# Kernel optimization log

Hardware: AMD Instinct MI355X
Metric: run time of the kernel (lower is better)

The kernel has to match this reference:

```python
import jax, jax.numpy as jnp
import numpy as np

HEIGHT = 8  # output crop height (module init arg)


def setup_inputs() -> dict:
    key = jax.random.key(0)
    k = jax.random.split(key, 8)
    N, Himg, Wimg, C = 16, 512, 512, 3
    M = 8192  # total boxes across the batch
    images = jax.random.normal(k[0], (N, Himg, Wimg, C), jnp.float32)
    feature_map = jax.random.normal(k[1], (N, 128, 128, 32), jnp.float32)
    # boxes: (x1, y1, x2, y2, angle); sized so width = HEIGHT*bw/bh <= 60 < max_width=64
    x1 = jax.random.uniform(k[2], (M,), minval=0.0, maxval=392.0)
    y1 = jax.random.uniform(k[3], (M,), minval=0.0, maxval=448.0)
    bw = jax.random.uniform(k[4], (M,), minval=16.0, maxval=120.0)
    bh = jax.random.uniform(k[5], (M,), minval=16.0, maxval=64.0)
    ang = jax.random.uniform(k[6], (M,), minval=-0.785, maxval=0.785)
    boxes = jnp.stack([x1, y1, x1 + bw, y1 + bh, ang], axis=-1)
    box_indices = jax.random.randint(k[7], (M,), 0, N).astype(jnp.int32)
    return {"images": images, "feature_map": feature_map, "boxes": boxes,
            "box_indices": box_indices, "max_width": 64}


def _roi_rotate(images, boxes, box_indices, max_width):
    """Rotated crop-and-resize with bilinear sampling.
    Returns crops [M, HEIGHT, max_width, C] (zero-padded past each box's width)
    and the per-box float output widths [M]."""
    Himg, Wimg = images.shape[1], images.shape[2]
    x1, y1, x2, y2, ang = (boxes[:, i] for i in range(5))
    bw, bh = x2 - x1, y2 - y1
    width = HEIGHT * bw / bh                      # per-box output width (float)
    cx, cy = (x1 + x2) * 0.5, (y1 + y2) * 0.5     # box center
    s = (bh / HEIGHT)[:, None, None]              # uniform scale (src px per dst px)

    ii = jnp.arange(HEIGHT, dtype=images.dtype)[None, :, None]      # [1,H,1]
    jj = jnp.arange(max_width, dtype=images.dtype)[None, None, :]   # [1,1,W]
    w_ = width[:, None, None]
    dx = s * (jj - (w_ - 1.0) * 0.5)              # [M,H,W] local offsets
    dy = s * (ii - (HEIGHT - 1.0) * 0.5)
    ca = jnp.cos(ang)[:, None, None]
    sa = jnp.sin(ang)[:, None, None]
    sx = cx[:, None, None] + ca * dx - sa * dy    # rotated source coords
    sy = cy[:, None, None] + sa * dx + ca * dy

    x0 = jnp.floor(sx)
    y0 = jnp.floor(sy)
    fx = (sx - x0)[..., None]
    fy = (sy - y0)[..., None]
    x0i = jnp.clip(x0, 0, Wimg - 1).astype(jnp.int32)
    x1i = jnp.clip(x0 + 1.0, 0, Wimg - 1).astype(jnp.int32)
    y0i = jnp.clip(y0, 0, Himg - 1).astype(jnp.int32)
    y1i = jnp.clip(y0 + 1.0, 0, Himg - 1).astype(jnp.int32)

    b = box_indices[:, None, None]                # [M,1,1] broadcasts to [M,H,W]
    v00 = images[b, y0i, x0i]                     # [M,H,W,C] irregular gathers
    v01 = images[b, y0i, x1i]
    v10 = images[b, y1i, x0i]
    v11 = images[b, y1i, x1i]
    out = (v00 * (1 - fx) * (1 - fy) + v01 * fx * (1 - fy)
           + v10 * (1 - fx) * fy + v11 * fx * fy)

    # zero outside the image and past each box's actual width (padding)
    valid = ((jj < jnp.ceil(w_)) & (sx >= 0) & (sx <= Wimg - 1)
             & (sy >= 0) & (sy <= Himg - 1))
    crops = out * valid[..., None].astype(out.dtype)
    return crops, width


def reference(images, feature_map, boxes, box_indices, max_width):
    # feature_map is accepted (forward signature) but, per the source, crops
    # are taken from `images`.
    crops, width = _roi_rotate(images, boxes, box_indices, max_width)
    boxes_padded_width = max_width - width
    return crops, boxes_padded_width
```

## Files before the change

kernel.cpp:

```cpp
#include <hip/hip_runtime.h>

#define HEIGHT 8

__global__ void __launch_bounds__(512)
roi_rotate_kernel(const float* __restrict__ images,
                  const float* __restrict__ boxes,
                  const int* __restrict__ box_indices,
                  float* __restrict__ crops,
                  float* __restrict__ width_out,
                  int max_width, int Himg, int Wimg)
{
    const int m   = blockIdx.x;
    const int tid = threadIdx.x;
    const int mw  = max_width;

    const float x1  = boxes[m * 5 + 0];
    const float y1  = boxes[m * 5 + 1];
    const float x2  = boxes[m * 5 + 2];
    const float y2  = boxes[m * 5 + 3];
    const float ang = boxes[m * 5 + 4];
    const float bwd = x2 - x1, bhd = y2 - y1;
    const float width = (float)HEIGHT * bwd / bhd;
    const float cx = (x1 + x2) * 0.5f;
    const float cy = (y1 + y2) * 0.5f;
    const float s  = bhd / (float)HEIGHT;
    const float ca = cosf(ang);
    const float sa = sinf(ang);

    if (tid == 0) width_out[m] = (float)mw - width;

    const int i = tid & (HEIGHT - 1);
    const int j = tid >> 3;

    const float dx = s * ((float)j - (width - 1.0f) * 0.5f);
    const float dy = s * ((float)i - ((float)HEIGHT - 1.0f) * 0.5f);
    const float sx = cx + ca * dx - sa * dy;
    const float sy = cy + sa * dx + ca * dy;

    float v0 = 0.0f, v1 = 0.0f, v2 = 0.0f;

    const bool valid = ((float)j < ceilf(width)) &&
                       (sx >= 0.0f) && (sx <= (float)(Wimg - 1)) &&
                       (sy >= 0.0f) && (sy <= (float)(Himg - 1));

    if (valid) {
        const float x0 = floorf(sx);
        const float y0 = floorf(sy);
        const float fx = sx - x0;
        const float fy = sy - y0;
        const int x0i = (int)fminf(fmaxf(x0,        0.0f), (float)(Wimg - 1));
        const int x1i = (int)fminf(fmaxf(x0 + 1.0f, 0.0f), (float)(Wimg - 1));
        const int y0i = (int)fminf(fmaxf(y0,        0.0f), (float)(Himg - 1));
        const int y1i = (int)fminf(fmaxf(y0 + 1.0f, 0.0f), (float)(Himg - 1));

        const int b = box_indices[m];
        const float* img = images + (size_t)b * Himg * Wimg * 3;
        const size_t o00 = ((size_t)y0i * Wimg + x0i) * 3;
        const size_t o01 = ((size_t)y0i * Wimg + x1i) * 3;
        const size_t o10 = ((size_t)y1i * Wimg + x0i) * 3;
        const size_t o11 = ((size_t)y1i * Wimg + x1i) * 3;

        const float w00 = (1.0f - fx) * (1.0f - fy);
        const float w01 = fx * (1.0f - fy);
        const float w10 = (1.0f - fx) * fy;
        const float w11 = fx * fy;

        v0 = img[o00 + 0] * w00 + img[o01 + 0] * w01 +
             img[o10 + 0] * w10 + img[o11 + 0] * w11;
        v1 = img[o00 + 1] * w00 + img[o01 + 1] * w01 +
             img[o10 + 1] * w10 + img[o11 + 1] * w11;
        v2 = img[o00 + 2] * w00 + img[o01 + 2] * w01 +
             img[o10 + 2] * w10 + img[o11 + 2] * w11;
    }

    __shared__ float lds[HEIGHT * (64 * 3 + 4)];
    const int STRIDE = 3 * mw + 4;
    float* dst = &lds[i * STRIDE + j * 3];
    dst[0] = v0; dst[1] = v1; dst[2] = v2;
    __syncthreads();

    float* oblk = crops + (size_t)m * HEIGHT * mw * 3;
    if ((mw & 3) == 0) {
        const int nf4 = (HEIGHT * mw * 3) >> 2;
        if (tid < nf4) {
            const int f   = tid * 4;
            const int ii  = f / (3 * mw);
            const int rem = f - ii * (3 * mw);
            const float4 val = *(const float4*)&lds[ii * STRIDE + rem];
            *(float4*)&oblk[f] = val;
        }
    } else {
        float* o = oblk + ((size_t)i * mw + j) * 3;
        o[0] = v0; o[1] = v1; o[2] = v2;
    }
}

extern "C" void kernel_launch(void* const* d_in, const int* in_sizes, int n_in,
                              void* d_out, int out_size, void* d_ws, size_t ws_size,
                              hipStream_t stream) {
    const float* images      = (const float*)d_in[0];
    const float* boxes       = (const float*)d_in[2];
    const int*   box_indices = (const int*)d_in[3];

    const int M  = in_sizes[3];
    const int mw = (out_size - M) / (M * HEIGHT * 3);
    const int Himg = 512, Wimg = 512;

    float* crops     = (float*)d_out;
    float* width_out = crops + (size_t)M * HEIGHT * mw * 3;

    dim3 block(HEIGHT * mw);
    dim3 grid(M);
    roi_rotate_kernel<<<grid, block, 0, stream>>>(images, boxes, box_indices,
                                                  crops, width_out, mw, Himg, Wimg);
}
```

Baseline: 37.79 us.

## Compute two rows per thread and load adjacent bilinear pixels as 6-float segments

Each thread now computes two output rows, which halves the block size to 256 threads, and the store loop becomes strided. The two horizontally adjacent texels are fetched as one 6-float struct per image row, replacing twelve scalar loads with two wider loads. Clamping is simplified because valid samples are already inside the image bounds. This targets load instruction count and per-thread overhead, at the cost of more registers per thread and less thread-level parallelism for hiding gather latency.

New measurement: 56.12 us. 1.49x slower.

```diff
diff --git a/kernel.cpp b/kernel.cpp
--- a/kernel.cpp
+++ b/kernel.cpp
@@ -2,7 +2,9 @@
 
 #define HEIGHT 8
 
-__global__ void __launch_bounds__(512)
+struct __attribute__((aligned(4))) Seg6 { float p[6]; };
+
+__global__ void __launch_bounds__(256)
 roi_rotate_kernel(const float* __restrict__ images,
                   const float* __restrict__ boxes,
                   const int* __restrict__ box_indices,
@@ -13,6 +15,9 @@
     const int m   = blockIdx.x;
     const int tid = threadIdx.x;
     const int mw  = max_width;
+    const int tpc = HEIGHT / 2;
+    const int j   = tid / tpc;
+    const int i0  = (tid - j * tpc) * 2;
 
     const float x1  = boxes[m * 5 + 0];
     const float y1  = boxes[m * 5 + 1];
@@ -26,72 +31,81 @@
     const float s  = bhd / (float)HEIGHT;
     const float ca = cosf(ang);
     const float sa = sinf(ang);
-
     if (tid == 0) width_out[m] = (float)mw - width;
 
-    const int i = tid & (HEIGHT - 1);
-    const int j = tid >> 3;
+    const int b = box_indices[m];
+    const float* img = images + (size_t)b * Himg * Wimg * 3;
 
-    const float dx = s * ((float)j - (width - 1.0f) * 0.5f);
-    const float dy = s * ((float)i - ((float)HEIGHT - 1.0f) * 0.5f);
-    const float sx = cx + ca * dx - sa * dy;
-    const float sy = cy + sa * dx + ca * dy;
+    const float dx   = s * ((float)j - (width - 1.0f) * 0.5f);
+    const float wlim = ceilf(width);
+    const bool  jok  = ((float)j < wlim);
 
-    float v0 = 0.0f, v1 = 0.0f, v2 = 0.0f;
+    float v[2][3] = {{0.f, 0.f, 0.f}, {0.f, 0.f, 0.f}};
 
-    const bool valid = ((float)j < ceilf(width)) &&
-                       (sx >= 0.0f) && (sx <= (float)(Wimg - 1)) &&
-                       (sy >= 0.0f) && (sy <= (float)(Himg - 1));
+    #pragma unroll
+    for (int t = 0; t < 2; ++t) {
+        const int   i  = i0 + t;
+        const float dy = s * ((float)i - ((float)HEIGHT - 1.0f) * 0.5f);
+        const float sx = cx + ca * dx - sa * dy;
+        const float sy = cy + sa * dx + ca * dy;
+        const bool valid = jok &&
+                           (sx >= 0.0f) && (sx <= (float)(Wimg - 1)) &&
+                           (sy >= 0.0f) && (sy <= (float)(Himg - 1));
+        if (!valid) continue;
 
-    if (valid) {
         const float x0 = floorf(sx);
         const float y0 = floorf(sy);
         const float fx = sx - x0;
         const float fy = sy - y0;
-        const int x0i = (int)fminf(fmaxf(x0,        0.0f), (float)(Wimg - 1));
-        const int x1i = (int)fminf(fmaxf(x0 + 1.0f, 0.0f), (float)(Wimg - 1));
-        const int y0i = (int)fminf(fmaxf(y0,        0.0f), (float)(Himg - 1));
-        const int y1i = (int)fminf(fmaxf(y0 + 1.0f, 0.0f), (float)(Himg - 1));
+        const int x0i = (int)x0;
+        const int y0i = (int)y0;
+        const int y1i = min(y0i + 1, Himg - 1);
+        const int xb  = min(x0i, Wimg - 2);
+        const int off0 = (x0i - xb) * 3;
+        const int off1 = (min(x0i + 1, Wimg - 1) - xb) * 3;
 
-        const int b = box_indices[m];
-        const float* img = images + (size_t)b * Himg * Wimg * 3;
-        const size_t o00 = ((size_t)y0i * Wimg + x0i) * 3;
-        const size_t o01 = ((size_t)y0i * Wimg + x1i) * 3;
-        const size_t o10 = ((size_t)y1i * Wimg + x0i) * 3;
-        const size_t o11 = ((size_t)y1i * Wimg + x1i) * 3;
+        const float* r0 = img + ((size_t)y0i * Wimg + xb) * 3;
+        const float* r1 = img + ((size_t)y1i * Wimg + xb) * 3;
+        const Seg6 s0 = *(const Seg6*)r0;
+        const Seg6 s1 = *(const Seg6*)r1;
 
         const float w00 = (1.0f - fx) * (1.0f - fy);
         const float w01 = fx * (1.0f - fy);
         const float w10 = (1.0f - fx) * fy;
         const float w11 = fx * fy;
 
-        v0 = img[o00 + 0] * w00 + img[o01 + 0] * w01 +
-             img[o10 + 0] * w10 + img[o11 + 0] * w11;
-        v1 = img[o00 + 1] * w00 + img[o01 + 1] * w01 +
-             img[o10 + 1] * w10 + img[o11 + 1] * w11;
-        v2 = img[o00 + 2] * w00 + img[o01 + 2] * w01 +
-             img[o10 + 2] * w10 + img[o11 + 2] * w11;
+        #pragma unroll
+        for (int c = 0; c < 3; ++c) {
+            v[t][c] = s0.p[off0 + c] * w00 + s0.p[off1 + c] * w01 +
+                      s1.p[off0 + c] * w10 + s1.p[off1 + c] * w11;
+        }
     }
 
-    __shared__ float lds[HEIGHT * (64 * 3 + 4)];
-    const int STRIDE = 3 * mw + 4;
-    float* dst = &lds[i * STRIDE + j * 3];
-    dst[0] = v0; dst[1] = v1; dst[2] = v2;
-    __syncthreads();
+    __shared__ float lds[HEIGHT * (3 * 64 + 4)];
+    float* oblk = crops + (size_t)m * HEIGHT * mw * 3;
 
-    float* oblk = crops + (size_t)m * HEIGHT * mw * 3;
-    if ((mw & 3) == 0) {
+    if (mw <= 64 && (mw & 3) == 0) {
+        const int STRIDE = 3 * mw + 4;
+        #pragma unroll
+        for (int t = 0; t < 2; ++t) {
+            float* dst = &lds[(i0 + t) * STRIDE + j * 3];
+            dst[0] = v[t][0]; dst[1] = v[t][1]; dst[2] = v[t][2];
+        }
+        __syncthreads();
         const int nf4 = (HEIGHT * mw * 3) >> 2;
-        if (tid < nf4) {
-            const int f   = tid * 4;
+        for (int t4 = tid; t4 < nf4; t4 += blockDim.x) {
+            const int f   = t4 * 4;
             const int ii  = f / (3 * mw);
             const int rem = f - ii * (3 * mw);
             const float4 val = *(const float4*)&lds[ii * STRIDE + rem];
             *(float4*)&oblk[f] = val;
         }
     } else {
-        float* o = oblk + ((size_t)i * mw + j) * 3;
-        o[0] = v0; o[1] = v1; o[2] = v2;
+        #pragma unroll
+        for (int t = 0; t < 2; ++t) {
+            float* o = oblk + ((size_t)(i0 + t) * mw + j) * 3;
+            o[0] = v[t][0]; o[1] = v[t][1]; o[2] = v[t][2];
+        }
     }
 }
 
@@ -109,7 +123,7 @@
     float* crops     = (float*)d_out;
     float* width_out = crops + (size_t)M * HEIGHT * mw * 3;
 
-    dim3 block(HEIGHT * mw);
+    dim3 block((HEIGHT / 2) * mw);
     dim3 grid(M);
     roi_rotate_kernel<<<grid, block, 0, stream>>>(images, boxes, box_indices,
                                                   crops, width_out, mw, Himg, Wimg);
```

## Remap threads row-major, load bilinear neighbors as contiguous pairs, drop LDS staging

Applied to the files above, without the earlier changes.

Threads are now mapped row-major (i = tid/mw, j = tid%mw), so adjacent threads write adjacent output pixels. Each pixel's two horizontal neighbors are fetched as one contiguous 24-byte chunk per image row, with clamping folded into the base index and fractional weight. The LDS transpose and float4 store path are removed in favor of direct strided 3-float stores. The aim is fewer load instructions and no barrier, but the stores become scalar rather than vectorized.

After: 37.12 us. About the same (-1.8%).

```diff
diff --git a/kernel.cpp b/kernel.cpp
--- a/kernel.cpp
+++ b/kernel.cpp
@@ -13,6 +13,8 @@
     const int m   = blockIdx.x;
     const int tid = threadIdx.x;
     const int mw  = max_width;
+    const int i   = tid / mw;
+    const int j   = tid - i * mw;
 
     const float x1  = boxes[m * 5 + 0];
     const float y1  = boxes[m * 5 + 1];
@@ -26,11 +28,7 @@
     const float s  = bhd / (float)HEIGHT;
     const float ca = cosf(ang);
     const float sa = sinf(ang);
-
     if (tid == 0) width_out[m] = (float)mw - width;
-
-    const int i = tid & (HEIGHT - 1);
-    const int j = tid >> 3;
 
     const float dx = s * ((float)j - (width - 1.0f) * 0.5f);
     const float dy = s * ((float)i - ((float)HEIGHT - 1.0f) * 0.5f);
@@ -46,53 +44,35 @@
     if (valid) {
         const float x0 = floorf(sx);
         const float y0 = floorf(sy);
-        const float fx = sx - x0;
-        const float fy = sy - y0;
-        const int x0i = (int)fminf(fmaxf(x0,        0.0f), (float)(Wimg - 1));
-        const int x1i = (int)fminf(fmaxf(x0 + 1.0f, 0.0f), (float)(Wimg - 1));
-        const int y0i = (int)fminf(fmaxf(y0,        0.0f), (float)(Himg - 1));
-        const int y1i = (int)fminf(fmaxf(y0 + 1.0f, 0.0f), (float)(Himg - 1));
+        const int x0i = (int)x0;
+        const int y0i = (int)y0;
+
+        const int xb = min(x0i, Wimg - 2);
+        const int yb = min(y0i, Himg - 2);
+        const float fx = (x0i == xb) ? (sx - x0) : 1.0f;
+        const float fy = (y0i == yb) ? (sy - y0) : 1.0f;
 
         const int b = box_indices[m];
         const float* img = images + (size_t)b * Himg * Wimg * 3;
-        const size_t o00 = ((size_t)y0i * Wimg + x0i) * 3;
-        const size_t o01 = ((size_t)y0i * Wimg + x1i) * 3;
-        const size_t o10 = ((size_t)y1i * Wimg + x0i) * 3;
-        const size_t o11 = ((size_t)y1i * Wimg + x1i) * 3;
+        const float* r0 = img + ((size_t)yb * Wimg + xb) * 3;
+        const float* r1 = r0 + (size_t)Wimg * 3;
+
+        float s0[6], s1[6];
+        __builtin_memcpy(s0, r0, 24);
+        __builtin_memcpy(s1, r1, 24);
 
         const float w00 = (1.0f - fx) * (1.0f - fy);
         const float w01 = fx * (1.0f - fy);
         const float w10 = (1.0f - fx) * fy;
         const float w11 = fx * fy;
 
-        v0 = img[o00 + 0] * w00 + img[o01 + 0] * w01 +
-             img[o10 + 0] * w10 + img[o11 + 0] * w11;
-        v1 = img[o00 + 1] * w00 + img[o01 + 1] * w01 +
-             img[o10 + 1] * w10 + img[o11 + 1] * w11;
-        v2 = img[o00 + 2] * w00 + img[o01 + 2] * w01 +
-             img[o10 + 2] * w10 + img[o11 + 2] * w11;
+        v0 = s0[0] * w00 + s0[3] * w01 + s1[0] * w10 + s1[3] * w11;
+        v1 = s0[1] * w00 + s0[4] * w01 + s1[1] * w10 + s1[4] * w11;
+        v2 = s0[2] * w00 + s0[5] * w01 + s1[2] * w10 + s1[5] * w11;
     }
 
-    __shared__ float lds[HEIGHT * (64 * 3 + 4)];
-    const int STRIDE = 3 * mw + 4;
-    float* dst = &lds[i * STRIDE + j * 3];
-    dst[0] = v0; dst[1] = v1; dst[2] = v2;
-    __syncthreads();
-
-    float* oblk = crops + (size_t)m * HEIGHT * mw * 3;
-    if ((mw & 3) == 0) {
-        const int nf4 = (HEIGHT * mw * 3) >> 2;
-        if (tid < nf4) {
-            const int f   = tid * 4;
-            const int ii  = f / (3 * mw);
-            const int rem = f - ii * (3 * mw);
-            const float4 val = *(const float4*)&lds[ii * STRIDE + rem];
-            *(float4*)&oblk[f] = val;
-        }
-    } else {
-        float* o = oblk + ((size_t)i * mw + j) * 3;
-        o[0] = v0; o[1] = v1; o[2] = v2;
-    }
+    float* o = crops + ((size_t)(m * HEIGHT + i) * mw + j) * 3;
+    o[0] = v0; o[1] = v1; o[2] = v2;
 }
 
 extern "C" void kernel_launch(void* const* d_in, const int* in_sizes, int n_in,
```
